# Optimization experiments

Measured on AMD Instinct MI355X. Metric: run time of the kernel, lower is better.

Reference implementation:

```python
import jax, jax.numpy as jnp
import numpy as np

N_NODES = 50000


def _deg_norm(idx, n):
    # DGL GraphConv norm='both': deg.clamp(min=1) ** -0.5
    deg = jax.ops.segment_sum(jnp.ones(idx.shape, jnp.float32), idx, num_segments=n)
    return jnp.clip(deg, 1.0, None) ** -0.5


def _gconv(x, src, dst, W, b, n):
    # h_i = (sum_{j->i} x_j / sqrt(dout_j * din_i)) @ W + b
    h = x * _deg_norm(src, n)[:, None]
    m = jax.ops.segment_sum(h[src], dst, num_segments=n)  # [N, F] SpMM
    m = m * _deg_norm(dst, n)[:, None]
    return m @ W + b


def _gcn3(x, src, dst, W1, b1, W2, b2, W3, b3, n):
    x = jax.nn.relu(_gconv(x, src, dst, W1, b1, n))
    x = jax.nn.relu(_gconv(x, src, dst, W2, b2, n))
    x = jax.nn.relu(_gconv(x, src, dst, W3, b3, n))
    return x


def setup_inputs() -> dict:
    key = jax.random.key(0)
    ks = jax.random.split(key, 16)
    N, E, F_IN, H = N_NODES, 800000, 128, 304
    inp = {}
    for i in range(4):
        inp[f"x{i+1}"] = jax.random.normal(ks[i], (N, F_IN), dtype=jnp.float32)
        inp[f"src{i+1}"] = jax.random.randint(ks[4 + 2 * i], (E,), 0, N, dtype=jnp.int32)
        inp[f"dst{i+1}"] = jax.random.randint(ks[5 + 2 * i], (E,), 0, N, dtype=jnp.int32)
    inp["W1"] = jax.random.normal(ks[12], (F_IN, H), dtype=jnp.float32) / np.sqrt(F_IN)
    inp["b1"] = jnp.zeros((H,), jnp.float32)
    inp["W2"] = jax.random.normal(ks[13], (H, H), dtype=jnp.float32) / np.sqrt(H)
    inp["b2"] = jnp.zeros((H,), jnp.float32)
    inp["W3"] = jax.random.normal(ks[14], (H, H), dtype=jnp.float32) / np.sqrt(H)
    inp["b3"] = jnp.zeros((H,), jnp.float32)
    return inp


def reference(x1, x2, x3, x4, src1, dst1, src2, dst2, src3, dst3, src4, dst4,
              W1, b1, W2, b2, W3, b3):
    n = N_NODES
    h1 = _gcn3(x1, src1, dst1, W1, b1, W2, b2, W3, b3, n)
    h2 = _gcn3(x2, src2, dst2, W1, b1, W2, b2, W3, b3, n)
    h3 = _gcn3(x3, src3, dst3, W1, b1, W2, b2, W3, b3, n)
    h4 = _gcn3(x4, src4, dst4, W1, b1, W2, b2, W3, b3, n)
    # multi_graph_opt='mean': mean over concatenated node axis -> [H]
    x = jnp.mean(jnp.concatenate([h1, h2, h3, h4], axis=0), axis=0)
    # output_opt='mean': scalar
    return jnp.mean(x)
```

## Files before the change

kernel.cpp:

```cpp
#include <hip/hip_runtime.h>
#include <hip/hip_bf16.h>


#define NN 50000
#define EN 800000
#define PEN 950000
#define NCH 64
#define CHE 12500
#define PBS 50016
#define SCB 49
#define DCH 13
#define DCN 4096

typedef unsigned int uint;
typedef unsigned short ushort;
typedef unsigned char uchar;
typedef short s8v __attribute__((ext_vector_type(8)));
typedef float f4v __attribute__((ext_vector_type(4)));
typedef float f2v __attribute__((ext_vector_type(2)));
typedef uint u4v __attribute__((ext_vector_type(4)));

__device__ inline ushort f2bf(float f) {
    uint u = __float_as_uint(f);
    uint r = (u + 0x7FFFu + ((u >> 16) & 1u)) >> 16;
    return (ushort)r;
}
__device__ inline uint pk2(float lo, float hi) {
    return (uint)f2bf(lo) | ((uint)f2bf(hi) << 16);
}
__device__ inline f4v mfma16(s8v a, s8v b, f4v c) {
    return __builtin_amdgcn_mfma_f32_16x16x32_bf16(a, b, c, 0, 0, 0);
}
__device__ inline uchar f2fp8(float f) {
    return (uchar)(__builtin_amdgcn_cvt_pk_fp8_f32(f, 0.f, 0, false) & 0xFF);
}
__device__ inline void acc16(u4v d, f2v* a) {
    a[0] += __builtin_amdgcn_cvt_pk_f32_fp8(d.x, false);
    a[1] += __builtin_amdgcn_cvt_pk_f32_fp8(d.x, true);
    a[2] += __builtin_amdgcn_cvt_pk_f32_fp8(d.y, false);
    a[3] += __builtin_amdgcn_cvt_pk_f32_fp8(d.y, true);
    a[4] += __builtin_amdgcn_cvt_pk_f32_fp8(d.z, false);
    a[5] += __builtin_amdgcn_cvt_pk_f32_fp8(d.z, true);
    a[6] += __builtin_amdgcn_cvt_pk_f32_fp8(d.w, false);
    a[7] += __builtin_amdgcn_cvt_pk_f32_fp8(d.w, true);
}

struct GP { const int* p[4]; };
struct FP { const float* p[4]; };


__global__ __launch_bounds__(256) void hist_kernel(GP src, GP dst,
                                                   uint* __restrict__ partS,
                                                   uint* __restrict__ partD) {
    int b = blockIdx.x, dir = blockIdx.y, g = blockIdx.z;
    const int* idx = dir ? dst.p[g] : src.p[g];
    __shared__ uint lh[PBS / 4];
    for (int i = threadIdx.x; i < PBS / 4; i += 256) lh[i] = 0;
    __syncthreads();
    int e0 = b * CHE;
    for (int e = e0 + threadIdx.x; e < e0 + CHE; e += 256) {
        uint n = (uint)idx[e];
        atomicAdd(&lh[n >> 2], 1u << (8 * (n & 3)));
    }
    __syncthreads();
    uint* out = (dir ? partD : partS) + (size_t)(g * NCH + b) * (PBS / 4);
    for (int i = threadIdx.x; i < PBS / 4; i += 256) out[i] = lh[i];
}

__global__ __launch_bounds__(256) void reduce_kernel(const uchar* __restrict__ partS,
                                                     uchar* __restrict__ partD,
                                                     float* __restrict__ ns,
                                                     float* __restrict__ nd,
                                                     int* __restrict__ degd) {
    int idx = blockIdx.x * 256 + threadIdx.x;
    if (idx >= 4 * NN) return;
    int g = idx / NN, n = idx - g * NN;
    const uchar* ps = partS + (size_t)(g * NCH) * PBS + n;
    uint ss = 0;
    for (int b = 0; b < NCH; b++) ss += ps[(size_t)b * PBS];
    uchar* pd = partD + (size_t)(g * NCH) * PBS + n;
    uint run = 0;
    for (int b = 0; b < NCH; b++) {
        uint v = pd[(size_t)b * PBS];
        pd[(size_t)b * PBS] = (uchar)run;
        run += v;
    }
    ns[idx] = rsqrtf((float)max(ss, 1u));
    nd[idx] = rsqrtf((float)max(run, 1u));
    degd[idx] = (int)run;
}

__global__ __launch_bounds__(1024) void scan1_kernel(const int* __restrict__ degd,
                                                     int* __restrict__ rs_all,
                                                     int* __restrict__ bsum) {
    int j = blockIdx.x, g = blockIdx.y;
    int i = j * 1024 + threadIdx.x;
    int v = (i < NN) ? ((degd[g * NN + i] + 3) & ~3) : 0;
    int lane = threadIdx.x & 63, w = threadIdx.x >> 6;
    int x = v;
    #pragma unroll
    for (int off = 1; off < 64; off <<= 1) {
        int t = __shfl_up(x, off, 64);
        if (lane >= off) x += t;
    }
    __shared__ int ws[17];
    if (lane == 63) ws[w] = x;
    __syncthreads();
    if (threadIdx.x == 0) {
        int run = 0;
        #pragma unroll
        for (int k = 0; k < 16; k++) { int t = ws[k]; ws[k] = run; run += t; }
        ws[16] = run;
    }
    __syncthreads();
    if (i < NN) rs_all[g * (NN + 1) + i] = ws[w] + x - v;
    if (threadIdx.x == 0) bsum[g * SCB + j] = ws[16];
}

__global__ void scan2_kernel(int* __restrict__ bsum, int* __restrict__ rs_all) {
    int g = threadIdx.x >> 6, lane = threadIdx.x & 63;
    int v = (lane < SCB) ? bsum[g * SCB + lane] : 0;
    int x = v;
    #pragma unroll
    for (int off = 1; off < 64; off <<= 1) {
        int t = __shfl_up(x, off, 64);
        if (lane >= off) x += t;
    }
    if (lane < SCB) bsum[g * SCB + lane] = x - v;
    if (lane == 63) rs_all[g * (NN + 1) + NN] = x;
}

__global__ __launch_bounds__(1024) void scan3_kernel(const int* __restrict__ bsum,
                                                     int* __restrict__ rs_all) {
    int j = blockIdx.x, g = blockIdx.y;
    int i = j * 1024 + threadIdx.x;
    int off = bsum[g * SCB + j];
    if (i < NN) rs_all[g * (NN + 1) + i] += off;
}

__global__ __launch_bounds__(256) void cfill_kernel(uint* __restrict__ csr2) {
    int i = blockIdx.x * 256 + threadIdx.x;
    if (i < 4 * PEN / 2) csr2[i] = (uint)NN | ((uint)NN << 16);
}

__global__ __launch_bounds__(256) void scatter_kernel(GP src, GP dst,
                                                      const int* __restrict__ rs_all,
                                                      const uchar* __restrict__ pf,
                                                      ushort* __restrict__ csr) {
    int b = blockIdx.x, g = blockIdx.y;
    __shared__ uint lc[PBS / 4];
    for (int i = threadIdx.x; i < PBS / 4; i += 256) lc[i] = 0;
    __syncthreads();
    const int* sp = src.p[g];
    const int* dp = dst.p[g];
    const int* rs = rs_all + g * (NN + 1);
    const uchar* pfb = pf + (size_t)(g * NCH + b) * PBS;
    ushort* csrg = csr + (size_t)g * PEN;
    int e0 = b * CHE;
    for (int e = e0 + threadIdx.x; e < e0 + CHE; e += 256) {
        uint d = (uint)dp[e];
        int s = sp[e];
        uint sh = 8 * (d & 3);
        uint old = atomicAdd(&lc[d >> 2], 1u << sh);
        uint r = (old >> sh) & 0xFFu;
        csrg[rs[d] + (int)pfb[d] + (int)r] = (ushort)s;
    }
}


__global__ __launch_bounds__(256) void dhist_kernel(const int* __restrict__ degd,
                                                    int* __restrict__ dhp) {
    int b = blockIdx.x, g = blockIdx.y;
    __shared__ int lh[256];
    lh[threadIdx.x] = 0;
    __syncthreads();
    int n0 = b * DCN, nend = min(n0 + DCN, NN);
    for (int i = n0 + threadIdx.x; i < nend; i += 256) {
        int d = degd[g * NN + i];
        atomicAdd(&lh[d < 255 ? d : 255], 1);
    }
    __syncthreads();
    dhp[(g * DCH + b) * 256 + threadIdx.x] = lh[threadIdx.x];
}

__global__ void dscan_kernel(int* __restrict__ dhp, int* __restrict__ dbase) {
    int tid = threadIdx.x, lane = tid & 63, w = tid >> 6;
    __shared__ int ws[4];
    for (int g = 0; g < 4; g++) {
        int run = 0;
        for (int c = 0; c < DCH; c++) {
            int v = dhp[(g * DCH + c) * 256 + tid];
            dhp[(g * DCH + c) * 256 + tid] = run;
            run += v;
        }
        int x = run;
        #pragma unroll
        for (int off = 1; off < 64; off <<= 1) {
            int t = __shfl_up(x, off, 64);
            if (lane >= off) x += t;
        }
        if (lane == 63) ws[w] = x;
        __syncthreads();
        int prefix = 0;
        for (int j = 0; j < w; j++) prefix += ws[j];
        dbase[g * 256 + tid] = prefix + x - run;
        __syncthreads();
    }
}

__global__ __launch_bounds__(256) void dscatter_kernel(const int* __restrict__ degd,
                                                       const int* __restrict__ dhp,
                                                       const int* __restrict__ dbase,
                                                       int* __restrict__ perm) {
    int b = blockIdx.x, g = blockIdx.y;
    __shared__ int lc[256];
    lc[threadIdx.x] = 0;
    __syncthreads();
    int n0 = b * DCN, nend = min(n0 + DCN, NN);
    for (int i = n0 + threadIdx.x; i < nend; i += 256) {
        int d = degd[g * NN + i];
        d = d < 255 ? d : 255;
        int r = atomicAdd(&lc[d], 1);
        int pos = dbase[g * 256 + d] + dhp[(g * DCH + b) * 256 + d] + r;
        perm[g * NN + pos] = i;
    }
}


__global__ void padzero_kernel(uint* __restrict__ xs, int nxs,
                               uint* __restrict__ hb, int nhb) {
    int t = threadIdx.x;
    if (t < nxs * 16) xs[(size_t)(t >> 4) * (NN + 1) * 16 + (size_t)NN * 16 + (t & 15)] = 0;
    if (t < nhb * 16) hb[(size_t)(t >> 4) * (NN + 1) * 16 + (size_t)NN * 16 + (t & 15)] = 0;
}


__global__ __launch_bounds__(256) void wtrans_kernel(const float* __restrict__ W,
                                                     ushort* __restrict__ Wt,
                                                     int Kreal, int WS) {
    int idx = blockIdx.x * 256 + threadIdx.x;
    if (idx >= 320 * WS) return;
    int n = idx / WS, k = idx - n * WS;
    float v = (n < 304 && k < Kreal) ? W[k * 304 + n] : 0.f;
    Wt[idx] = f2bf(v);
}


__global__ __launch_bounds__(256) void prescale_kernel(FP xp,
                                                       const float* __restrict__ ns,
                                                       uint* __restrict__ xs) {
    int g = blockIdx.y;
    const float* x = xp.p[g];
    ns += (size_t)g * NN;
    xs += (size_t)g * 2 * (NN + 1) * 16;
    int idx = blockIdx.x * 256 + threadIdx.x;
    if (idx >= NN * 16) return;
    int row = idx >> 4, j = idx & 15;
    int sl = j >> 3, pos = j & 7;
    float nv = ns[row];
    float4 v0 = ((const float4*)x)[idx * 2];
    float4 v1 = ((const float4*)x)[idx * 2 + 1];
    int p0 = 0, p1 = 0;
    p0 = __builtin_amdgcn_cvt_pk_fp8_f32(v0.x * nv, v0.y * nv, p0, false);
    p0 = __builtin_amdgcn_cvt_pk_fp8_f32(v0.z * nv, v0.w * nv, p0, true);
    p1 = __builtin_amdgcn_cvt_pk_fp8_f32(v1.x * nv, v1.y * nv, p1, false);
    p1 = __builtin_amdgcn_cvt_pk_fp8_f32(v1.z * nv, v1.w * nv, p1, true);
    ((uint2*)xs)[(size_t)sl * (NN + 1) * 8 + row * 8 + pos] = make_uint2((uint)p0, (uint)p1);
}

__global__ __launch_bounds__(256) void spmm_kernel(const u4v* __restrict__ xsl,
                                                   const int* __restrict__ prs,
                                                   const ushort* __restrict__ csr,
                                                   const float* __restrict__ nd,
                                                   const int* __restrict__ perm,
                                                   u4v* __restrict__ out,
                                                   int ostride) {
    int g = blockIdx.z, SL = gridDim.y;
    xsl += (size_t)g * SL * (NN + 1) * 4;
    prs += (size_t)g * (NN + 1);
    csr += (size_t)g * PEN;
    nd  += (size_t)g * NN;
    perm += (size_t)g * NN;
    out += (size_t)g * NN * ostride;

    int wv = threadIdx.x >> 6, lane = threadIdx.x & 63;
    int grp = lane >> 2, gl = lane & 3;
    int slot = blockIdx.x * 64 + wv * 16 + grp;
    int sl = blockIdx.y;
    const u4v* base = xsl + (size_t)sl * (NN + 1) * 4 + gl;
    bool ok = slot < NN;
    int node = ok ? perm[slot] : 0;
    int p0 = ok ? prs[node] : 0, p1 = ok ? prs[node + 1] : 0;
    f2v a[8];
    #pragma unroll
    for (int i = 0; i < 8; i++) a[i] = (f2v){0.f, 0.f};
    for (int e = p0; e < p1; e += 4) {
        uint2 e4 = *(const uint2*)(csr + e);
        uint s0 = e4.x & 0xFFFFu, s1 = e4.x >> 16;
        uint s2 = e4.y & 0xFFFFu, s3 = e4.y >> 16;
        u4v d0 = base[s0 * 4];
        u4v d1 = base[s1 * 4];
        u4v d2 = base[s2 * 4];
        u4v d3 = base[s3 * 4];
        acc16(d0, a); acc16(d1, a); acc16(d2, a); acc16(d3, a);
    }
    if (ok) {
        float nv = nd[node];
        f2v nv2 = {nv, nv};
        f2v c0 = a[0] * nv2, c1 = a[1] * nv2, c2 = a[2] * nv2, c3 = a[3] * nv2;
        f2v c4 = a[4] * nv2, c5 = a[5] * nv2, c6 = a[6] * nv2, c7 = a[7] * nv2;
        u4v o0, o1;
        o0.x = pk2(c0[0], c0[1]); o0.y = pk2(c1[0], c1[1]);
        o0.z = pk2(c2[0], c2[1]); o0.w = pk2(c3[0], c3[1]);
        o1.x = pk2(c4[0], c4[1]); o1.y = pk2(c5[0], c5[1]);
        o1.z = pk2(c6[0], c6[1]); o1.w = pk2(c7[0], c7[1]);
        u4v* op = out + (size_t)node * ostride + sl * 8 + gl * 2;
        __builtin_nontemporal_store(o0, op);
        __builtin_nontemporal_store(o1, op + 1);
    }
}


template<int KSTEPS, bool REDUCE>
__global__ __launch_bounds__(256) void gemm_kernel(const ushort* __restrict__ A, int astride,
                                                   const ushort* __restrict__ Wt,
                                                   const float* __restrict__ bias,
                                                   const float* __restrict__ ns,
                                                   uchar* __restrict__ Hout,
                                                   double* __restrict__ accum,
                                                   int M) {
    constexpr int K = KSTEPS * 32;
    constexpr int WS = K + 8;
    __shared__ __align__(16) ushort wt[80 * WS];
    __shared__ float redbuf[4];
    int g = blockIdx.z;
    A += (size_t)g * NN * astride;
    int tid = threadIdx.x, lane = tid & 63, wv = tid >> 6;
    int nb = blockIdx.x * 80;
    int r0 = blockIdx.y * 128 + wv * 32;

    {
        const s8v* src = (const s8v*)(Wt + (size_t)nb * WS);
        s8v* dst = (s8v*)wt;
        for (int i = tid; i < 80 * WS / 8; i += 256) dst[i] = src[i];
    }
    __syncthreads();

    f4v acc[2][5];
    #pragma unroll
    for (int t = 0; t < 2; t++)
        #pragma unroll
        for (int j = 0; j < 5; j++) acc[t][j] = (f4v){0.f, 0.f, 0.f, 0.f};

    int m15 = lane & 15;
    int kq = (lane >> 4) * 8;
    int ar0 = min(r0 + m15, M - 1);
    int ar1 = min(r0 + 16 + m15, M - 1);
    const ushort* a0p = A + (size_t)ar0 * astride + kq;
    const ushort* a1p = A + (size_t)ar1 * astride + kq;
    const ushort* bb = wt + (size_t)m15 * WS + kq;

    #pragma unroll
    for (int ks = 0; ks < KSTEPS; ks++) {
        s8v af0 = *(const s8v*)(a0p + ks * 32);
        s8v af1 = *(const s8v*)(a1p + ks * 32);
        #pragma unroll
        for (int nt = 0; nt < 5; nt++) {
            s8v bf = *(const s8v*)(bb + nt * 16 * WS + ks * 32);
            acc[0][nt] = mfma16(af0, bf, acc[0][nt]);
            acc[1][nt] = mfma16(af1, bf, acc[1][nt]);
        }
    }

    int rq = (lane >> 4) * 4;
    if constexpr (!REDUCE) {
        const float* nsg = ns + (size_t)g * NN;
        uchar* hg = Hout + (size_t)g * 5 * (NN + 1) * 64;
        float nsv[2][4];
        #pragma unroll
        for (int t = 0; t < 2; t++)
            #pragma unroll
            for (int r = 0; r < 4; r++) {
                int row = r0 + t * 16 + rq + r;
                nsv[t][r] = (row < M) ? nsg[row] : 0.f;
            }
        #pragma unroll
        for (int nt = 0; nt < 5; nt++) {
            int col = nb + nt * 16 + m15;
            float bv = (col < 304) ? bias[col] : 0.f;
            int sl = col >> 6, cw = col & 63;
            uchar* hp = hg + (size_t)sl * (NN + 1) * 64 + cw;
            #pragma unroll
            for (int t = 0; t < 2; t++)
                #pragma unroll
                for (int r = 0; r < 4; r++) {
                    int row = r0 + t * 16 + rq + r;
                    if (row < M) {
                        float y = fmaxf(acc[t][nt][r] + bv, 0.f) * nsv[t][r];
                        hp[(size_t)row * 64] = f2fp8(y);
                    }
                }
        }
    } else {
        float s = 0.f;
        #pragma unroll
        for (int nt = 0; nt < 5; nt++) {
            int col = nb + nt * 16 + m15;
            float bv = (col < 304) ? bias[col] : 0.f;
            #pragma unroll
            for (int t = 0; t < 2; t++)
                #pragma unroll
                for (int r = 0; r < 4; r++) {
                    int row = r0 + t * 16 + rq + r;
                    if (row < M && col < 304) s += fmaxf(acc[t][nt][r] + bv, 0.f);
                }
        }
        #pragma unroll
        for (int off = 32; off; off >>= 1) s += __shfl_xor(s, off, 64);
        if (lane == 0) redbuf[wv] = s;
        __syncthreads();
        if (tid == 0) {
            double b = (double)redbuf[0] + redbuf[1] + redbuf[2] + redbuf[3];
            atomicAdd(accum, b);
        }
    }
}

__global__ void finalize_kernel(const double* __restrict__ accum, float* __restrict__ out) {
    out[0] = (float)(accum[0] / (double)(4.0 * NN * 304.0));
}


extern "C" void kernel_launch(void* const* d_in, const int* in_sizes, int n_in,
                              void* d_out, int out_size, void* d_ws, size_t ws_size,
                              hipStream_t stream) {
    char* w = (char*)d_ws;
    auto alloc = [&](size_t bytes) {
        char* p = w;
        w += (bytes + 255) & ~(size_t)255;
        return p;
    };
    double* accum  = (double*)alloc(256);
    int*    degd   = (int*)alloc((size_t)4 * NN * 4);
    int*    rs     = (int*)alloc((size_t)4 * (NN + 1) * 4);
    int*    bsum   = (int*)alloc((size_t)4 * SCB * 4);
    float*  nsrc   = (float*)alloc((size_t)4 * NN * 4);
    float*  ndst   = (float*)alloc((size_t)4 * NN * 4);
    ushort* csr    = (ushort*)alloc((size_t)4 * PEN * 2);
    int*    dhp    = (int*)alloc((size_t)4 * DCH * 256 * 4);
    int*    dbase  = (int*)alloc((size_t)4 * 256 * 4);
    int*    perm   = (int*)alloc((size_t)4 * NN * 4);
    ushort* wt1    = (ushort*)alloc((size_t)320 * 136 * 2);
    ushort* wt2    = (ushort*)alloc((size_t)320 * 328 * 2);
    ushort* wt3    = (ushort*)alloc((size_t)320 * 328 * 2);
    uint*   partS  = (uint*)alloc((size_t)4 * NCH * PBS);
    uint*   partD  = (uint*)alloc((size_t)4 * NCH * PBS);

    size_t need_tail = ((size_t)4 * 5 * (NN + 1) * 64 + 255 + (size_t)4 * NN * 320 * 2 + 255);
    size_t used = (size_t)(w - (char*)d_ws);
    bool batched = (ws_size >= used + need_tail + 4096);

    uint *hbuf, *mbuf, *xs, *m1;
    if (batched) {
        hbuf = (uint*)alloc((size_t)4 * 5 * (NN + 1) * 64);
        mbuf = (uint*)alloc((size_t)4 * NN * 320 * 2);
        xs   = partS;
        m1   = mbuf;
    } else {
        hbuf = (uint*)alloc((size_t)5 * (NN + 1) * 64);
        mbuf = (uint*)alloc((size_t)NN * 320 * 2);
        xs   = partS;
        m1   = partD;
    }

    (void)hipMemsetAsync(accum, 0, 256, stream);

    wtrans_kernel<<<(320 * 136 + 255) / 256, 256, 0, stream>>>((const float*)d_in[12], wt1, 128, 136);
    wtrans_kernel<<<(320 * 328 + 255) / 256, 256, 0, stream>>>((const float*)d_in[14], wt2, 304, 328);
    wtrans_kernel<<<(320 * 328 + 255) / 256, 256, 0, stream>>>((const float*)d_in[16], wt3, 304, 328);

    GP S, D;
    FP X;
    for (int g = 0; g < 4; g++) {
        S.p[g] = (const int*)d_in[1 + 3 * g];
        D.p[g] = (const int*)d_in[2 + 3 * g];
        X.p[g] = (const float*)d_in[3 * g];
    }
    hist_kernel<<<dim3(NCH, 2, 4), 256, 0, stream>>>(S, D, partS, partD);
    reduce_kernel<<<(4 * NN + 255) / 256, 256, 0, stream>>>((const uchar*)partS, (uchar*)partD,
                                                            nsrc, ndst, degd);
    scan1_kernel<<<dim3(SCB, 4), 1024, 0, stream>>>(degd, rs, bsum);
    scan2_kernel<<<1, 256, 0, stream>>>(bsum, rs);
    scan3_kernel<<<dim3(SCB, 4), 1024, 0, stream>>>(bsum, rs);
    cfill_kernel<<<(4 * PEN / 2 + 255) / 256, 256, 0, stream>>>((uint*)csr);
    scatter_kernel<<<dim3(NCH, 4), 256, 0, stream>>>(S, D, rs, (const uchar*)partD, csr);
    dhist_kernel<<<dim3(DCH, 4), 256, 0, stream>>>(degd, dhp);
    dscan_kernel<<<1, 256, 0, stream>>>(dhp, dbase);
    dscatter_kernel<<<dim3(DCH, 4), 256, 0, stream>>>(degd, dhp, dbase, perm);
    padzero_kernel<<<1, 512, 0, stream>>>(xs, batched ? 8 : 2, hbuf, batched ? 20 : 5);

    const float* b1 = (const float*)d_in[13];
    const float* b2 = (const float*)d_in[15];
    const float* b3 = (const float*)d_in[17];

    if (batched) {
        dim3 pgrid((NN * 16 + 255) / 256, 4);
        dim3 sgrid1((NN + 63) / 64, 2, 4);
        dim3 sgrid2((NN + 63) / 64, 5, 4);
        dim3 ggrid(4, (NN + 127) / 128, 4);
        prescale_kernel<<<pgrid, 256, 0, stream>>>(X, nsrc, xs);
        spmm_kernel<<<sgrid1, 256, 0, stream>>>((const u4v*)xs, rs, csr,
                                                ndst, perm, (u4v*)m1, 16);
        gemm_kernel<4, false><<<ggrid, 256, 0, stream>>>((const ushort*)m1, 128, wt1, b1, nsrc,
                                                         (uchar*)hbuf, nullptr, NN);
        spmm_kernel<<<sgrid2, 256, 0, stream>>>((const u4v*)hbuf, rs, csr,
                                                ndst, perm, (u4v*)mbuf, 40);
        gemm_kernel<10, false><<<ggrid, 256, 0, stream>>>((const ushort*)mbuf, 320, wt2, b2, nsrc,
                                                          (uchar*)hbuf, nullptr, NN);
        spmm_kernel<<<sgrid2, 256, 0, stream>>>((const u4v*)hbuf, rs, csr,
                                                ndst, perm, (u4v*)mbuf, 40);
        gemm_kernel<10, true><<<ggrid, 256, 0, stream>>>((const ushort*)mbuf, 320, wt3, b3, nullptr,
                                                         nullptr, accum, NN);
    } else {
        dim3 pgrid((NN * 16 + 255) / 256, 1);
        dim3 sgrid1((NN + 63) / 64, 2);
        dim3 sgrid2((NN + 63) / 64, 5);
        dim3 ggrid(4, (NN + 127) / 128);
        for (int g = 0; g < 4; g++) {
            FP Xg;
            Xg.p[0] = Xg.p[1] = Xg.p[2] = Xg.p[3] = (const float*)d_in[3 * g];
            const float* nsg = nsrc + g * NN;
            const float* ndg = ndst + g * NN;
            const int* rsg = rs + g * (NN + 1);
            const ushort* csrg = csr + (size_t)g * PEN;
            const int* permg = perm + g * NN;

            prescale_kernel<<<pgrid, 256, 0, stream>>>(Xg, nsg, xs);
            spmm_kernel<<<sgrid1, 256, 0, stream>>>((const u4v*)xs, rsg, csrg,
                                                    ndg, permg, (u4v*)m1, 16);
            gemm_kernel<4, false><<<ggrid, 256, 0, stream>>>((const ushort*)m1, 128, wt1, b1, nsg,
                                                             (uchar*)hbuf, nullptr, NN);
            spmm_kernel<<<sgrid2, 256, 0, stream>>>((const u4v*)hbuf, rsg, csrg,
                                                    ndg, permg, (u4v*)mbuf, 40);
            gemm_kernel<10, false><<<ggrid, 256, 0, stream>>>((const ushort*)mbuf, 320, wt2, b2, nsg,
                                                              (uchar*)hbuf, nullptr, NN);
            spmm_kernel<<<sgrid2, 256, 0, stream>>>((const u4v*)hbuf, rsg, csrg,
                                                    ndg, permg, (u4v*)mbuf, 40);
            gemm_kernel<10, true><<<ggrid, 256, 0, stream>>>((const ushort*)mbuf, 320, wt3, b3, nullptr,
                                                             nullptr, accum, NN);
        }
    }
    finalize_kernel<<<1, 1, 0, stream>>>(accum, (float*)d_out);
}
```

Before: 1.112 ms.

## Remap SpMM and GEMM block indices for XCD-aware L2 locality

Replaces the 3D grids of the SpMM and GEMM kernels with flat 1D grids. Block indices are decoded so that each group of consecutive blocks (b&7, matching the 8 XCDs on MI355X) is pinned to one feature slice or graph chunk, letting each XCD's L2 hold a smaller working set of gathered rows and weights. SpMM node ranges are split into halves/parts per slice-group. CSR index loads become nontemporal to avoid polluting cache. The risks are load imbalance across XCDs and the extra integer index arithmetic per block.

```diff
diff --git a/kernel.cpp b/kernel.cpp
--- a/kernel.cpp
+++ b/kernel.cpp
@@ -11,6 +11,7 @@
 #define SCB 49
 #define DCH 13
 #define DCN 4096
+#define CPG 391
 
 typedef unsigned int uint;
 typedef unsigned short ushort;
@@ -19,6 +20,7 @@
 typedef float f4v __attribute__((ext_vector_type(4)));
 typedef float f2v __attribute__((ext_vector_type(2)));
 typedef uint u4v __attribute__((ext_vector_type(4)));
+typedef uint u2v __attribute__((ext_vector_type(2)));
 
 __device__ inline ushort f2bf(float f) {
     uint u = __float_as_uint(f);
@@ -274,8 +276,15 @@
                                                    const float* __restrict__ nd,
                                                    const int* __restrict__ perm,
                                                    u4v* __restrict__ out,
-                                                   int ostride) {
-    int g = blockIdx.z, SL = gridDim.y;
+                                                   int ostride, int SL, int UH,
+                                                   int NPX, int HN, int NSG) {
+    int b = blockIdx.x;
+    int r = b & 7, k = b >> 3;
+    int hpl = k / UH, unit = k - hpl * UH;
+    int hp = hpl * 8 + r;
+    int slg = hp % NSG, h = hp / NSG;
+    int g = slg / SL, sl = slg - g * SL;
+
     xsl += (size_t)g * SL * (NN + 1) * 4;
     prs += (size_t)g * (NN + 1);
     csr += (size_t)g * PEN;
@@ -285,17 +294,17 @@
 
     int wv = threadIdx.x >> 6, lane = threadIdx.x & 63;
     int grp = lane >> 2, gl = lane & 3;
-    int slot = blockIdx.x * 64 + wv * 16 + grp;
-    int sl = blockIdx.y;
+    int slot = h * HN + unit * 64 + wv * 16 + grp;
+    int send = min(NN, h * HN + HN);
     const u4v* base = xsl + (size_t)sl * (NN + 1) * 4 + gl;
-    bool ok = slot < NN;
+    bool ok = slot < send;
     int node = ok ? perm[slot] : 0;
     int p0 = ok ? prs[node] : 0, p1 = ok ? prs[node + 1] : 0;
     f2v a[8];
     #pragma unroll
     for (int i = 0; i < 8; i++) a[i] = (f2v){0.f, 0.f};
     for (int e = p0; e < p1; e += 4) {
-        uint2 e4 = *(const uint2*)(csr + e);
+        u2v e4 = __builtin_nontemporal_load((const u2v*)(csr + e));
         uint s0 = e4.x & 0xFFFFu, s1 = e4.x >> 16;
         uint s2 = e4.y & 0xFFFFu, s3 = e4.y >> 16;
         u4v d0 = base[s0 * 4];
@@ -328,16 +337,23 @@
                                                    const float* __restrict__ ns,
                                                    uchar* __restrict__ Hout,
                                                    double* __restrict__ accum,
-                                                   int M) {
+                                                   int CH) {
     constexpr int K = KSTEPS * 32;
     constexpr int WS = K + 8;
+    int b = blockIdx.x;
+    int r = b & 7, k = b >> 3;
+    int cl = k >> 2, nt = k & 3;
+    int chunk = cl * 8 + r;
+    if (chunk >= CH) return;
+    int g = chunk / CPG, rc = chunk - g * CPG;
+    int M = NN;
+
     __shared__ __align__(16) ushort wt[80 * WS];
     __shared__ float redbuf[4];
-    int g = blockIdx.z;
     A += (size_t)g * NN * astride;
     int tid = threadIdx.x, lane = tid & 63, wv = tid >> 6;
-    int nb = blockIdx.x * 80;
-    int r0 = blockIdx.y * 128 + wv * 32;
+    int nb = nt * 80;
+    int r0 = rc * 128 + wv * 32;
 
     {
         const s8v* src = (const s8v*)(Wt + (size_t)nb * WS);
@@ -365,10 +381,10 @@
         s8v af0 = *(const s8v*)(a0p + ks * 32);
         s8v af1 = *(const s8v*)(a1p + ks * 32);
         #pragma unroll
-        for (int nt = 0; nt < 5; nt++) {
-            s8v bf = *(const s8v*)(bb + nt * 16 * WS + ks * 32);
-            acc[0][nt] = mfma16(af0, bf, acc[0][nt]);
-            acc[1][nt] = mfma16(af1, bf, acc[1][nt]);
+        for (int nt2 = 0; nt2 < 5; nt2++) {
+            s8v bf = *(const s8v*)(bb + nt2 * 16 * WS + ks * 32);
+            acc[0][nt2] = mfma16(af0, bf, acc[0][nt2]);
+            acc[1][nt2] = mfma16(af1, bf, acc[1][nt2]);
         }
     }
 
@@ -380,23 +396,23 @@
         #pragma unroll
         for (int t = 0; t < 2; t++)
             #pragma unroll
-            for (int r = 0; r < 4; r++) {
-                int row = r0 + t * 16 + rq + r;
-                nsv[t][r] = (row < M) ? nsg[row] : 0.f;
+            for (int rr = 0; rr < 4; rr++) {
+                int row = r0 + t * 16 + rq + rr;
+                nsv[t][rr] = (row < M) ? nsg[row] : 0.f;
             }
         #pragma unroll
-        for (int nt = 0; nt < 5; nt++) {
-            int col = nb + nt * 16 + m15;
+        for (int nt2 = 0; nt2 < 5; nt2++) {
+            int col = nb + nt2 * 16 + m15;
             float bv = (col < 304) ? bias[col] : 0.f;
             int sl = col >> 6, cw = col & 63;
             uchar* hp = hg + (size_t)sl * (NN + 1) * 64 + cw;
             #pragma unroll
             for (int t = 0; t < 2; t++)
                 #pragma unroll
-                for (int r = 0; r < 4; r++) {
-                    int row = r0 + t * 16 + rq + r;
+                for (int rr = 0; rr < 4; rr++) {
+                    int row = r0 + t * 16 + rq + rr;
                     if (row < M) {
-                        float y = fmaxf(acc[t][nt][r] + bv, 0.f) * nsv[t][r];
+                        float y = fmaxf(acc[t][nt2][rr] + bv, 0.f) * nsv[t][rr];
                         hp[(size_t)row * 64] = f2fp8(y);
                     }
                 }
@@ -404,15 +420,15 @@
     } else {
         float s = 0.f;
         #pragma unroll
-        for (int nt = 0; nt < 5; nt++) {
-            int col = nb + nt * 16 + m15;
+        for (int nt2 = 0; nt2 < 5; nt2++) {
+            int col = nb + nt2 * 16 + m15;
             float bv = (col < 304) ? bias[col] : 0.f;
             #pragma unroll
             for (int t = 0; t < 2; t++)
                 #pragma unroll
-                for (int r = 0; r < 4; r++) {
-                    int row = r0 + t * 16 + rq + r;
-                    if (row < M && col < 304) s += fmaxf(acc[t][nt][r] + bv, 0.f);
+                for (int rr = 0; rr < 4; rr++) {
+                    int row = r0 + t * 16 + rq + rr;
+                    if (row < M && col < 304) s += fmaxf(acc[t][nt2][rr] + bv, 0.f);
                 }
         }
         #pragma unroll
@@ -420,8 +436,8 @@
         if (lane == 0) redbuf[wv] = s;
         __syncthreads();
         if (tid == 0) {
-            double b = (double)redbuf[0] + redbuf[1] + redbuf[2] + redbuf[3];
-            atomicAdd(accum, b);
+            double bsum = (double)redbuf[0] + redbuf[1] + redbuf[2] + redbuf[3];
+            atomicAdd(accum, bsum);
         }
     }
 }
@@ -505,27 +521,27 @@
 
     if (batched) {
         dim3 pgrid((NN * 16 + 255) / 256, 4);
-        dim3 sgrid1((NN + 63) / 64, 2, 4);
-        dim3 sgrid2((NN + 63) / 64, 5, 4);
-        dim3 ggrid(4, (NN + 127) / 128, 4);
+        int B1 = 8 * 1 * 782;
+        int B2 = 8 * 5 * 391;
+        int BG = 8 * 196 * 4;
         prescale_kernel<<<pgrid, 256, 0, stream>>>(X, nsrc, xs);
-        spmm_kernel<<<sgrid1, 256, 0, stream>>>((const u4v*)xs, rs, csr,
-                                                ndst, perm, (u4v*)m1, 16);
-        gemm_kernel<4, false><<<ggrid, 256, 0, stream>>>((const ushort*)m1, 128, wt1, b1, nsrc,
-                                                         (uchar*)hbuf, nullptr, NN);
-        spmm_kernel<<<sgrid2, 256, 0, stream>>>((const u4v*)hbuf, rs, csr,
-                                                ndst, perm, (u4v*)mbuf, 40);
-        gemm_kernel<10, false><<<ggrid, 256, 0, stream>>>((const ushort*)mbuf, 320, wt2, b2, nsrc,
-                                                          (uchar*)hbuf, nullptr, NN);
-        spmm_kernel<<<sgrid2, 256, 0, stream>>>((const u4v*)hbuf, rs, csr,
-                                                ndst, perm, (u4v*)mbuf, 40);
-        gemm_kernel<10, true><<<ggrid, 256, 0, stream>>>((const ushort*)mbuf, 320, wt3, b3, nullptr,
-                                                         nullptr, accum, NN);
+        spmm_kernel<<<B1, 256, 0, stream>>>((const u4v*)xs, rs, csr, ndst, perm,
+                                            (u4v*)m1, 16, 2, 782, 1, NN, 8);
+        gemm_kernel<4, false><<<BG, 256, 0, stream>>>((const ushort*)m1, 128, wt1, b1, nsrc,
+                                                      (uchar*)hbuf, nullptr, 4 * CPG);
+        spmm_kernel<<<B2, 256, 0, stream>>>((const u4v*)hbuf, rs, csr, ndst, perm,
+                                            (u4v*)mbuf, 40, 5, 391, 5, 25000, 20);
+        gemm_kernel<10, false><<<BG, 256, 0, stream>>>((const ushort*)mbuf, 320, wt2, b2, nsrc,
+                                                       (uchar*)hbuf, nullptr, 4 * CPG);
+        spmm_kernel<<<B2, 256, 0, stream>>>((const u4v*)hbuf, rs, csr, ndst, perm,
+                                            (u4v*)mbuf, 40, 5, 391, 5, 25000, 20);
+        gemm_kernel<10, true><<<BG, 256, 0, stream>>>((const ushort*)mbuf, 320, wt3, b3, nullptr,
+                                                      nullptr, accum, 4 * CPG);
     } else {
         dim3 pgrid((NN * 16 + 255) / 256, 1);
-        dim3 sgrid1((NN + 63) / 64, 2);
-        dim3 sgrid2((NN + 63) / 64, 5);
-        dim3 ggrid(4, (NN + 127) / 128);
+        int B1 = 8 * 1 * 196;
+        int B2 = 8 * 5 * 98;
+        int BG = 8 * 49 * 4;
         for (int g = 0; g < 4; g++) {
             FP Xg;
             Xg.p[0] = Xg.p[1] = Xg.p[2] = Xg.p[3] = (const float*)d_in[3 * g];
@@ -536,18 +552,18 @@
             const int* permg = perm + g * NN;
 
             prescale_kernel<<<pgrid, 256, 0, stream>>>(Xg, nsg, xs);
-            spmm_kernel<<<sgrid1, 256, 0, stream>>>((const u4v*)xs, rsg, csrg,
-                                                    ndg, permg, (u4v*)m1, 16);
-            gemm_kernel<4, false><<<ggrid, 256, 0, stream>>>((const ushort*)m1, 128, wt1, b1, nsg,
-                                                             (uchar*)hbuf, nullptr, NN);
-            spmm_kernel<<<sgrid2, 256, 0, stream>>>((const u4v*)hbuf, rsg, csrg,
-                                                    ndg, permg, (u4v*)mbuf, 40);
-            gemm_kernel<10, false><<<ggrid, 256, 0, stream>>>((const ushort*)mbuf, 320, wt2, b2, nsg,
-                                                              (uchar*)hbuf, nullptr, NN);
-            spmm_kernel<<<sgrid2, 256, 0, stream>>>((const u4v*)hbuf, rsg, csrg,
-                                                    ndg, permg, (u4v*)mbuf, 40);
-            gemm_kernel<10, true><<<ggrid, 256, 0, stream>>>((const ushort*)mbuf, 320, wt3, b3, nullptr,
-                                                             nullptr, accum, NN);
+            spmm_kernel<<<B1, 256, 0, stream>>>((const u4v*)xs, rsg, csrg, ndg, permg,
+                                                (u4v*)m1, 16, 2, 196, 1, 12500, 2);
+            gemm_kernel<4, false><<<BG, 256, 0, stream>>>((const ushort*)m1, 128, wt1, b1, nsg,
+                                                          (uchar*)hbuf, nullptr, CPG);
+            spmm_kernel<<<B2, 256, 0, stream>>>((const u4v*)hbuf, rsg, csrg, ndg, permg,
+                                                (u4v*)mbuf, 40, 5, 98, 5, 6250, 5);
+            gemm_kernel<10, false><<<BG, 256, 0, stream>>>((const ushort*)mbuf, 320, wt2, b2, nsg,
+                                                           (uchar*)hbuf, nullptr, CPG);
+            spmm_kernel<<<B2, 256, 0, stream>>>((const u4v*)hbuf, rsg, csrg, ndg, permg,
+                                                (u4v*)mbuf, 40, 5, 98, 5, 6250, 5);
+            gemm_kernel<10, true><<<BG, 256, 0, stream>>>((const ushort*)mbuf, 320, wt3, b3, nullptr,
+                                                          nullptr, accum, CPG);
         }
     }
     finalize_kernel<<<1, 1, 0, stream>>>(accum, (float*)d_out);
```

New measurement: 1.139 ms. 2.4% more time.
